# Optimization experiments

Hardware: AMD Instinct MI355X
Metric: run time of the kernel (lower is better)

The kernel has to match this reference:

```python
import jax, jax.numpy as jnp
import numpy as np

GROUPS = 8
EPS = 1e-5


def group_norm(x, w, b, groups=GROUPS, eps=EPS):
    B, C, H, W = x.shape
    xg = x.reshape(B, groups, C // groups, H, W)
    mean = xg.mean(axis=(2, 3, 4), keepdims=True)
    var = xg.var(axis=(2, 3, 4), keepdims=True)
    xg = (xg - mean) * jax.lax.rsqrt(var + eps)
    x = xg.reshape(B, C, H, W)
    return x * w[None, :, None, None] + b[None, :, None, None]


def setup_inputs() -> dict:
    key = jax.random.key(0)
    ks = jax.random.split(key, 7)
    C = 512
    x = jax.random.normal(ks[0], (16, C, 32, 32), dtype=jnp.float32)
    norm_w = jnp.ones((C,), dtype=jnp.float32)
    norm_b = jnp.zeros((C,), dtype=jnp.float32)
    s = 1.0 / np.sqrt(C)
    qkv_w = jax.random.uniform(ks[1], (3 * C, C), jnp.float32, -s, s)
    qkv_b = jax.random.uniform(ks[2], (3 * C,), jnp.float32, -s, s)
    proj_w = jax.random.uniform(ks[3], (C, C), jnp.float32, -s, s)
    proj_b = jax.random.uniform(ks[4], (C,), jnp.float32, -s, s)
    return {"x": x, "norm_w": norm_w, "norm_b": norm_b, "qkv_w": qkv_w,
            "qkv_b": qkv_b, "proj_w": proj_w, "proj_b": proj_b}


def reference(x, norm_w, norm_b, qkv_w, qkv_b, proj_w, proj_b):
    B, C, H, W = x.shape
    h_in = x
    xn = group_norm(x, norm_w, norm_b)
    # 1x1 conv == per-pixel linear over channels
    qkv = jnp.einsum('oc,bchw->bohw', qkv_w, xn) + qkv_b[None, :, None, None]
    q, k, v = jnp.split(qkv, 3, axis=1)
    q = q.reshape(B, C, H * W)
    k = k.reshape(B, C, H * W)
    v = v.reshape(B, C, H * W)
    attn = jnp.einsum('bci,bcj->bij', q, k) / jnp.sqrt(jnp.asarray(C, x.dtype))
    attn = jax.nn.softmax(attn, axis=-1)
    out = jnp.einsum('bij,bcj->bci', attn, v).reshape(B, C, H, W)
    out = jnp.einsum('oc,bchw->bohw', proj_w, out) + proj_b[None, :, None, None]
    return h_in + out
```

## Files before the change

### kernel.cpp

```cpp
#include <hip/hip_runtime.h>
#include <stdint.h>

typedef __attribute__((ext_vector_type(4))) float f32x4;
typedef __attribute__((ext_vector_type(8))) __bf16 bf16x8;

__device__ __forceinline__ unsigned short f2bf(float f) {
  union { float f; unsigned u; } v; v.f = f;
  unsigned r = v.u + 0x7FFF + ((v.u >> 16) & 1);
  return (unsigned short)(r >> 16);
}

__device__ __forceinline__ void g2l16(const void* g, void* l) {
  __builtin_amdgcn_global_load_lds((const __attribute__((address_space(1))) void*)g,
                                   (__attribute__((address_space(3))) void*)l, 16, 0, 0);
}

__global__ void cvt_weights(const float* __restrict__ a, const float* __restrict__ p,
                            unsigned short* __restrict__ wa, unsigned short* __restrict__ wp) {
  int i = blockIdx.x * 256 + threadIdx.x;
  if (i < 786432) wa[i] = f2bf(a[i]);
  else wp[i - 786432] = f2bf(p[i - 786432]);
}

__global__ __launch_bounds__(256) void gn_fused(
    const float* __restrict__ x, const float* __restrict__ gw, const float* __restrict__ gb,
    unsigned short* __restrict__ xnT) {
  __shared__ float tile[64][65];
  __shared__ float red[8];
  __shared__ float mv[2];
  int bid = blockIdx.x;
  int g = bid & 7, b = bid >> 3;
  int t = threadIdx.x;
  const float4* p = (const float4*)(x + (size_t)bid * 65536);
  float s = 0.f, ss = 0.f;
  for (int i = t; i < 16384; i += 256) {
    float4 v = p[i];
    s += v.x + v.y + v.z + v.w;
    ss += v.x * v.x + v.y * v.y + v.z * v.z + v.w * v.w;
  }
#pragma unroll
  for (int o = 32; o > 0; o >>= 1) {
    s += __shfl_down(s, o, 64);
    ss += __shfl_down(ss, o, 64);
  }
  int w = t >> 6;
  if ((t & 63) == 0) { red[w] = s; red[4 + w] = ss; }
  __syncthreads();
  if (t == 0) {
    s = red[0] + red[1] + red[2] + red[3];
    ss = red[4] + red[5] + red[6] + red[7];
    float mean = s * (1.f / 65536.f);
    float var = ss * (1.f / 65536.f) - mean * mean;
    mv[0] = mean; mv[1] = rsqrtf(var + 1e-5f);
  }
  __syncthreads();
  float mean = mv[0], rstd = mv[1];
  const float* src = x + (size_t)bid * 65536;
  for (int ch = 0; ch < 16; ch++) {
#pragma unroll
    for (int i = 0; i < 4; i++) {
      int lin = t + i * 256;
      int c = lin >> 4, p4 = lin & 15;
      float4 v = *(const float4*)(src + (size_t)c * 1024 + ch * 64 + p4 * 4);
      float gg = gw[g * 64 + c] * rstd;
      float bb = gb[g * 64 + c] - mean * gg;
      tile[c][p4 * 4 + 0] = v.x * gg + bb;
      tile[c][p4 * 4 + 1] = v.y * gg + bb;
      tile[c][p4 * 4 + 2] = v.z * gg + bb;
      tile[c][p4 * 4 + 3] = v.w * gg + bb;
    }
    __syncthreads();
    unsigned short* dst = xnT + ((size_t)b * 1024 + ch * 64) * 512 + g * 64;
#pragma unroll
    for (int i = 0; i < 4; i++) {
      int lin = t + i * 256;
      int pp = lin >> 4, cq = lin & 15;
      ushort4 o;
      o.x = f2bf(tile[cq * 4 + 0][pp]);
      o.y = f2bf(tile[cq * 4 + 1][pp]);
      o.z = f2bf(tile[cq * 4 + 2][pp]);
      o.w = f2bf(tile[cq * 4 + 3][pp]);
      *(ushort4*)(dst + (size_t)pp * 512 + cq * 4) = o;
    }
    __syncthreads();
  }
}

template <int EPI, bool OUT_BF16>
__global__ __launch_bounds__(256) void gemm_bt(
    const unsigned short* __restrict__ A, int lda, long long sA,
    const unsigned short* __restrict__ B, int ldb, long long sB,
    void* __restrict__ Cv, int ldc, long long sC,
    const float* __restrict__ bias,
    const float* __restrict__ res, long long sRes,
    int M, int N, int K, int mt, int nt) {
  __shared__ __align__(16) unsigned short As[128 * 32];
  __shared__ __align__(16) unsigned short Bs[128 * 32];
  int bid = blockIdx.x;
  int per = mt * nt;
  int b = bid / per;
  int r = bid % per;
  int mi = r / nt, ni = r % nt;
  int t = threadIdx.x;
  int l = t & 63, w = t >> 6;
  int wm = w >> 1, wn = w & 1;
  int fr = l & 15;
  int fk = (l >> 4) << 3;
  const unsigned short* Ab = A + (size_t)b * sA + (size_t)(mi * 128) * lda;
  const unsigned short* Bb = B + (size_t)b * sB + (size_t)(ni * 128) * ldb;
  int sr = t >> 2, sk = (t & 3) << 3;
  const unsigned short* gA = Ab + (size_t)sr * lda + sk;
  const unsigned short* gB = Bb + (size_t)sr * ldb + sk;
  unsigned short* lA = As + w * 512;
  unsigned short* lB = Bs + w * 512;
  const unsigned short* ra = As + (wm * 64 + fr) * 32 + fk;
  const unsigned short* rb = Bs + (wn * 64 + fr) * 32 + fk;
  f32x4 acc[4][4] = {};
  for (int k0 = 0; k0 < K; k0 += 32) {
    g2l16(gA, lA);
    g2l16(gA + (size_t)64 * lda, lA + 2048);
    g2l16(gB, lB);
    g2l16(gB + (size_t)64 * ldb, lB + 2048);
    gA += 32; gB += 32;
    __syncthreads();
    bf16x8 af[4], bv[4];
#pragma unroll
    for (int i = 0; i < 4; i++) af[i] = *(const bf16x8*)(ra + i * 512);
#pragma unroll
    for (int j = 0; j < 4; j++) bv[j] = *(const bf16x8*)(rb + j * 512);
#pragma unroll
    for (int i = 0; i < 4; i++)
#pragma unroll
      for (int j = 0; j < 4; j++)
        acc[i][j] = __builtin_amdgcn_mfma_f32_16x16x32_bf16(af[i], bv[j], acc[i][j], 0, 0, 0);
    __syncthreads();
  }
  int crow0 = mi * 128 + wm * 64;
  int ccol0 = ni * 128 + wn * 64;
  int lr = (l >> 4) << 2;
  int lc = l & 15;
#pragma unroll
  for (int i = 0; i < 4; i++) {
#pragma unroll
    for (int j = 0; j < 4; j++) {
      int col = ccol0 + j * 16 + lc;
      float bn = (EPI == 1) ? bias[col] : 0.0f;
#pragma unroll
      for (int e = 0; e < 4; e++) {
        int row = crow0 + i * 16 + lr + e;
        float v = acc[i][j][e];
        if (EPI == 1) v += bn;
        if (EPI == 2 || EPI == 3) v += bias[row];
        if (EPI == 3) v += res[(size_t)b * sRes + (size_t)row * ldc + col];
        size_t o = (size_t)b * sC + (size_t)row * ldc + col;
        if (OUT_BF16) ((unsigned short*)Cv)[o] = f2bf(v);
        else ((float*)Cv)[o] = v;
      }
    }
  }
}

__global__ __launch_bounds__(512, 2) void flash_attn(
    const unsigned short* __restrict__ qkT, const unsigned short* __restrict__ vbuf,
    unsigned short* __restrict__ obuf) {
  __shared__ __align__(16) unsigned short Qs[64 * 520];
  __shared__ __align__(16) float Slds[64 * 132];
  __shared__ __align__(16) unsigned short Plds[4 * 64 * 40];
  __shared__ float mrow[64], lrow[64], scl[64];

  const float SC = 0.04419417382415922f;
  int bid = blockIdx.x;
  int logical = (bid & 7) * 32 + (bid >> 3);
  int b = logical >> 4, it = logical & 15;
  int i0 = it * 64;
  int tid = threadIdx.x;
  int l = tid & 63, w = tid >> 6;
  int fr = l & 15, fq = l >> 4;
  int d0 = w * 64;

  const size_t bq = (size_t)b * 1048576;
  const size_t bv = (size_t)b * 524288;

  {
    const unsigned short* qsrc = qkT + bq + (size_t)i0 * 1024 + l * 8;
#pragma unroll
    for (int i = 0; i < 8; i++) {
      int row = i * 8 + w;
      g2l16(qsrc + (size_t)row * 1024, (char*)Qs + row * 1040);
    }
  }
  if (tid < 64) { mrow[tid] = -3e38f; lrow[tid] = 0.f; }
  __syncthreads();

  f32x4 acc[4][4] = {};
  const unsigned short* kg = qkT + bq + 512 + (size_t)(w * 16 + fr) * 1024 + fq * 8;
  const unsigned short* vg = vbuf + bv + (size_t)(d0 + fr) * 1024 + fq * 8;

  int smr = w * 8 + (l & 7);
  int sm8 = l >> 3;

#pragma unroll 1
  for (int jt = 0; jt < 8; jt++) {
    const unsigned short* kgj = kg + (size_t)jt * 131072;
    bf16x8 kf[16];
#pragma unroll
    for (int ks = 0; ks < 16; ks++) kf[ks] = *(const bf16x8*)(kgj + ks * 32);
    const unsigned short* vgj = vg + jt * 128;
    bf16x8 vf[16];
#pragma unroll
    for (int nj = 0; nj < 4; nj++)
#pragma unroll
      for (int kp = 0; kp < 4; kp++)
        vf[nj * 4 + kp] = *(const bf16x8*)(vgj + nj * 16384 + kp * 32);

    {
      f32x4 sacc[4] = {};
#pragma unroll
      for (int ks = 0; ks < 16; ks++) {
#pragma unroll
        for (int mi = 0; mi < 4; mi++) {
          bf16x8 qa = *(const bf16x8*)((const char*)Qs + (mi * 16 + fr) * 1040 + (ks * 4 + fq) * 16);
          sacc[mi] = __builtin_amdgcn_mfma_f32_16x16x32_bf16(qa, kf[ks], sacc[mi], 0, 0, 0);
        }
      }
#pragma unroll
      for (int mi = 0; mi < 4; mi++) {
        float* sp = Slds + (mi * 16 + fq * 4) * 132 + w * 16 + fr;
#pragma unroll
        for (int e = 0; e < 4; e++) sp[e * 132] = sacc[mi][e];
      }
    }
    asm volatile("s_waitcnt lgkmcnt(0)" ::: "memory");
    __builtin_amdgcn_s_barrier();
    __builtin_amdgcn_sched_barrier(0);

    {
      int r = smr, s8 = sm8;
      const float* srowp = Slds + r * 132 + s8 * 16;
      float4 a0 = *(const float4*)(srowp + 0);
      float4 a1 = *(const float4*)(srowp + 4);
      float4 a2 = *(const float4*)(srowp + 8);
      float4 a3 = *(const float4*)(srowp + 12);
      float mx = fmaxf(fmaxf(fmaxf(a0.x, a0.y), fmaxf(a0.z, a0.w)),
                       fmaxf(fmaxf(a1.x, a1.y), fmaxf(a1.z, a1.w)));
      mx = fmaxf(mx, fmaxf(fmaxf(fmaxf(a2.x, a2.y), fmaxf(a2.z, a2.w)),
                           fmaxf(fmaxf(a3.x, a3.y), fmaxf(a3.z, a3.w))));
      mx = fmaxf(mx, __shfl_xor(mx, 8, 64));
      mx = fmaxf(mx, __shfl_xor(mx, 16, 64));
      mx = fmaxf(mx, __shfl_xor(mx, 32, 64));
      float mold = mrow[r];
      float mnew = fmaxf(mold, mx);
      float e0 = __expf((a0.x - mnew) * SC), e1 = __expf((a0.y - mnew) * SC);
      float e2 = __expf((a0.z - mnew) * SC), e3 = __expf((a0.w - mnew) * SC);
      float e4 = __expf((a1.x - mnew) * SC), e5 = __expf((a1.y - mnew) * SC);
      float e6 = __expf((a1.z - mnew) * SC), e7 = __expf((a1.w - mnew) * SC);
      float e8 = __expf((a2.x - mnew) * SC), e9 = __expf((a2.y - mnew) * SC);
      float ea = __expf((a2.z - mnew) * SC), eb = __expf((a2.w - mnew) * SC);
      float ec = __expf((a3.x - mnew) * SC), ed = __expf((a3.y - mnew) * SC);
      float ee = __expf((a3.z - mnew) * SC), ef = __expf((a3.w - mnew) * SC);
      float sum = ((e0 + e1) + (e2 + e3)) + ((e4 + e5) + (e6 + e7)) +
                  ((e8 + e9) + (ea + eb)) + ((ec + ed) + (ee + ef));
      sum += __shfl_xor(sum, 8, 64);
      sum += __shfl_xor(sum, 16, 64);
      sum += __shfl_xor(sum, 32, 64);
      uint4 pw0, pw1;
      pw0.x = f2bf(e0) | ((unsigned)f2bf(e1) << 16);
      pw0.y = f2bf(e2) | ((unsigned)f2bf(e3) << 16);
      pw0.z = f2bf(e4) | ((unsigned)f2bf(e5) << 16);
      pw0.w = f2bf(e6) | ((unsigned)f2bf(e7) << 16);
      pw1.x = f2bf(e8) | ((unsigned)f2bf(e9) << 16);
      pw1.y = f2bf(ea) | ((unsigned)f2bf(eb) << 16);
      pw1.z = f2bf(ec) | ((unsigned)f2bf(ed) << 16);
      pw1.w = f2bf(ee) | ((unsigned)f2bf(ef) << 16);
      char* pp = (char*)Plds + (s8 >> 1) * 5120 + r * 80 + (s8 & 1) * 32;
      *(uint4*)pp = pw0;
      *(uint4*)(pp + 16) = pw1;
      if (s8 == 0) {
        float sf = __expf((mold - mnew) * SC);
        lrow[r] = lrow[r] * sf + sum;
        mrow[r] = mnew;
        scl[r] = sf;
      }
    }
    asm volatile("s_waitcnt lgkmcnt(0)" ::: "memory");
    __builtin_amdgcn_s_barrier();
    __builtin_amdgcn_sched_barrier(0);

    {
      f32x4 sc4[4];
#pragma unroll
      for (int mi = 0; mi < 4; mi++) sc4[mi] = *(const f32x4*)(scl + mi * 16 + fq * 4);
#pragma unroll
      for (int mi = 0; mi < 4; mi++)
#pragma unroll
        for (int nj = 0; nj < 4; nj++) acc[mi][nj] *= sc4[mi];
#pragma unroll
      for (int kp = 0; kp < 4; kp++) {
        bf16x8 pf[4];
#pragma unroll
        for (int mi = 0; mi < 4; mi++)
          pf[mi] = *(const bf16x8*)((const char*)Plds + kp * 5120 + (mi * 16 + fr) * 80 + fq * 16);
#pragma unroll
        for (int nj = 0; nj < 4; nj++) {
#pragma unroll
          for (int mi = 0; mi < 4; mi++)
            acc[mi][nj] = __builtin_amdgcn_mfma_f32_16x16x32_bf16(pf[mi], vf[nj * 4 + kp], acc[mi][nj], 0, 0, 0);
        }
      }
    }
  }

  f32x4 linv[4];
#pragma unroll
  for (int mi = 0; mi < 4; mi++) {
    f32x4 lv = *(const f32x4*)(lrow + mi * 16 + fq * 4);
#pragma unroll
    for (int e = 0; e < 4; e++) linv[mi][e] = 1.0f / lv[e];
  }
  unsigned short* ob = obuf + bv + (size_t)i0 * 512 + d0 + fr;
#pragma unroll
  for (int mi = 0; mi < 4; mi++)
#pragma unroll
    for (int nj = 0; nj < 4; nj++)
#pragma unroll
      for (int e = 0; e < 4; e++) {
        int row = mi * 16 + fq * 4 + e;
        ob[(size_t)row * 512 + nj * 16] = f2bf(acc[mi][nj][e] * linv[mi][e]);
      }
}

extern "C" void kernel_launch(void* const* d_in, const int* in_sizes, int n_in,
                              void* d_out, int out_size, void* d_ws, size_t ws_size,
                              hipStream_t stream) {
  const float* x = (const float*)d_in[0];
  const float* norm_w = (const float*)d_in[1];
  const float* norm_b = (const float*)d_in[2];
  const float* qkv_w = (const float*)d_in[3];
  const float* qkv_b = (const float*)d_in[4];
  const float* proj_w = (const float*)d_in[5];
  const float* proj_b = (const float*)d_in[6];
  float* out = (float*)d_out;
  char* ws = (char*)d_ws;

  size_t off = 0;
  auto alloc = [&](size_t bytes) {
    off = (off + 255) & ~(size_t)255;
    size_t r = off; off += bytes; return r;
  };
  unsigned short* wqkv  = (unsigned short*)(ws + alloc((size_t)1536 * 512 * 2));
  unsigned short* wproj = (unsigned short*)(ws + alloc((size_t)512 * 512 * 2));
  unsigned short* xnT   = (unsigned short*)(ws + alloc((size_t)16 * 1024 * 512 * 2));
  unsigned short* qkT   = (unsigned short*)(ws + alloc((size_t)16 * 1024 * 1024 * 2));
  unsigned short* vbuf  = (unsigned short*)(ws + alloc((size_t)16 * 512 * 1024 * 2));
  unsigned short* obuf  = (unsigned short*)(ws + alloc((size_t)16 * 1024 * 512 * 2));

  cvt_weights<<<4096, 256, 0, stream>>>(qkv_w, proj_w, wqkv, wproj);
  gn_fused<<<128, 256, 0, stream>>>(x, norm_w, norm_b, xnT);

  gemm_bt<1, true><<<1024, 256, 0, stream>>>(
      xnT, 512, 1024LL * 512, wqkv, 512, 0,
      qkT, 1024, 1024LL * 1024, qkv_b, nullptr, 0, 1024, 1024, 512, 8, 8);

  gemm_bt<2, true><<<512, 256, 0, stream>>>(
      wqkv + (size_t)1024 * 512, 512, 0, xnT, 512, 1024LL * 512,
      vbuf, 1024, 512LL * 1024, qkv_b + 1024, nullptr, 0, 512, 1024, 512, 4, 8);

  flash_attn<<<256, 512, 0, stream>>>(qkT, vbuf, obuf);

  gemm_bt<3, false><<<512, 256, 0, stream>>>(
      wproj, 512, 0, obuf, 512, 1024LL * 512,
      out, 1024, 512LL * 1024, proj_b, x, 512LL * 1024, 512, 1024, 512, 4, 8);
}
```

Baseline: 285.3 us.

## Compute flash-attention softmax in registers with per-wave max/sum tables

The softmax no longer goes through an fp32 score tile in LDS. Each wave reduces row maxima and row sums of its own MFMA score fragments with cross-lane shuffles and publishes partials to small double-buffered LDS tables, while running max and sum stay in registers. P is written to LDS directly from the fragments, and the V loads are issued before the K loads. This removes the fp32 score round trip through LDS and the separate softmax thread mapping, at the cost of more shuffles and some redundant exponentials and table reads per lane.

```diff
diff --git a/kernel.cpp b/kernel.cpp
--- a/kernel.cpp
+++ b/kernel.cpp
@@ -164,9 +164,9 @@
     const unsigned short* __restrict__ qkT, const unsigned short* __restrict__ vbuf,
     unsigned short* __restrict__ obuf) {
   __shared__ __align__(16) unsigned short Qs[64 * 520];
-  __shared__ __align__(16) float Slds[64 * 132];
-  __shared__ __align__(16) unsigned short Plds[4 * 64 * 40];
-  __shared__ float mrow[64], lrow[64], scl[64];
+  __shared__ __align__(16) unsigned short Plds[2][64 * 136];
+  __shared__ __align__(16) float mtab[2][8][64];
+  __shared__ __align__(16) float ltab[2][8][64];
 
   const float SC = 0.04419417382415922f;
   int bid = blockIdx.x;
@@ -189,144 +189,136 @@
       g2l16(qsrc + (size_t)row * 1024, (char*)Qs + row * 1040);
     }
   }
-  if (tid < 64) { mrow[tid] = -3e38f; lrow[tid] = 0.f; }
   __syncthreads();
 
   f32x4 acc[4][4] = {};
+  f32x4 mrun[4], lrun[4];
+#pragma unroll
+  for (int mi = 0; mi < 4; mi++) {
+    mrun[mi] = f32x4{-3e38f, -3e38f, -3e38f, -3e38f};
+    lrun[mi] = f32x4{0.f, 0.f, 0.f, 0.f};
+  }
+
   const unsigned short* kg = qkT + bq + 512 + (size_t)(w * 16 + fr) * 1024 + fq * 8;
   const unsigned short* vg = vbuf + bv + (size_t)(d0 + fr) * 1024 + fq * 8;
 
-  int smr = w * 8 + (l & 7);
-  int sm8 = l >> 3;
-
 #pragma unroll 1
   for (int jt = 0; jt < 8; jt++) {
+    int buf = jt & 1;
+    const unsigned short* vgj = vg + jt * 128;
+    bf16x8 vf[16];
+#pragma unroll
+    for (int nj = 0; nj < 4; nj++)
+#pragma unroll
+      for (int kp = 0; kp < 4; kp++)
+        vf[nj * 4 + kp] = *(const bf16x8*)(vgj + nj * 16384 + kp * 32);
+    __builtin_amdgcn_sched_barrier(0);
+
     const unsigned short* kgj = kg + (size_t)jt * 131072;
     bf16x8 kf[16];
 #pragma unroll
     for (int ks = 0; ks < 16; ks++) kf[ks] = *(const bf16x8*)(kgj + ks * 32);
-    const unsigned short* vgj = vg + jt * 128;
-    bf16x8 vf[16];
-#pragma unroll
-    for (int nj = 0; nj < 4; nj++)
-#pragma unroll
-      for (int kp = 0; kp < 4; kp++)
-        vf[nj * 4 + kp] = *(const bf16x8*)(vgj + nj * 16384 + kp * 32);
-
-    {
-      f32x4 sacc[4] = {};
-#pragma unroll
-      for (int ks = 0; ks < 16; ks++) {
-#pragma unroll
-        for (int mi = 0; mi < 4; mi++) {
-          bf16x8 qa = *(const bf16x8*)((const char*)Qs + (mi * 16 + fr) * 1040 + (ks * 4 + fq) * 16);
-          sacc[mi] = __builtin_amdgcn_mfma_f32_16x16x32_bf16(qa, kf[ks], sacc[mi], 0, 0, 0);
-        }
-      }
+    f32x4 sacc[4] = {};
+#pragma unroll
+    for (int ks = 0; ks < 16; ks++) {
 #pragma unroll
       for (int mi = 0; mi < 4; mi++) {
-        float* sp = Slds + (mi * 16 + fq * 4) * 132 + w * 16 + fr;
-#pragma unroll
-        for (int e = 0; e < 4; e++) sp[e * 132] = sacc[mi][e];
-      }
+        bf16x8 qa = *(const bf16x8*)((const char*)Qs + (mi * 16 + fr) * 1040 + (ks * 4 + fq) * 16);
+        sacc[mi] = __builtin_amdgcn_mfma_f32_16x16x32_bf16(qa, kf[ks], sacc[mi], 0, 0, 0);
+      }
+    }
+
+#pragma unroll
+    for (int mi = 0; mi < 4; mi++) {
+      f32x4 v = sacc[mi];
+#pragma unroll
+      for (int mask = 1; mask < 16; mask <<= 1)
+#pragma unroll
+        for (int e = 0; e < 4; e++) v[e] = fmaxf(v[e], __shfl_xor(v[e], mask, 64));
+      if (fr == 0) *(f32x4*)&mtab[buf][w][mi * 16 + fq * 4] = v;
     }
     asm volatile("s_waitcnt lgkmcnt(0)" ::: "memory");
     __builtin_amdgcn_s_barrier();
     __builtin_amdgcn_sched_barrier(0);
 
+    f32x4 alpha[4];
+#pragma unroll
+    for (int mi = 0; mi < 4; mi++) {
+      f32x4 mm = mrun[mi];
+#pragma unroll
+      for (int s = 0; s < 8; s++) {
+        f32x4 ms = *(const f32x4*)&mtab[buf][s][mi * 16 + fq * 4];
+#pragma unroll
+        for (int e = 0; e < 4; e++) mm[e] = fmaxf(mm[e], ms[e]);
+      }
+#pragma unroll
+      for (int e = 0; e < 4; e++) alpha[mi][e] = __expf((mrun[mi][e] - mm[e]) * SC);
+      f32x4 p;
+#pragma unroll
+      for (int e = 0; e < 4; e++) p[e] = __expf((sacc[mi][e] - mm[e]) * SC);
+      sacc[mi] = p;
+      mrun[mi] = mm;
+      f32x4 sum = p;
+#pragma unroll
+      for (int mask = 1; mask < 16; mask <<= 1)
+#pragma unroll
+        for (int e = 0; e < 4; e++) sum[e] += __shfl_xor(sum[e], mask, 64);
+      if (fr == 0) *(f32x4*)&ltab[buf][w][mi * 16 + fq * 4] = sum;
+    }
     {
-      int r = smr, s8 = sm8;
-      const float* srowp = Slds + r * 132 + s8 * 16;
-      float4 a0 = *(const float4*)(srowp + 0);
-      float4 a1 = *(const float4*)(srowp + 4);
-      float4 a2 = *(const float4*)(srowp + 8);
-      float4 a3 = *(const float4*)(srowp + 12);
-      float mx = fmaxf(fmaxf(fmaxf(a0.x, a0.y), fmaxf(a0.z, a0.w)),
-                       fmaxf(fmaxf(a1.x, a1.y), fmaxf(a1.z, a1.w)));
-      mx = fmaxf(mx, fmaxf(fmaxf(fmaxf(a2.x, a2.y), fmaxf(a2.z, a2.w)),
-                           fmaxf(fmaxf(a3.x, a3.y), fmaxf(a3.z, a3.w))));
-      mx = fmaxf(mx, __shfl_xor(mx, 8, 64));
-      mx = fmaxf(mx, __shfl_xor(mx, 16, 64));
-      mx = fmaxf(mx, __shfl_xor(mx, 32, 64));
-      float mold = mrow[r];
-      float mnew = fmaxf(mold, mx);
-      float e0 = __expf((a0.x - mnew) * SC), e1 = __expf((a0.y - mnew) * SC);
-      float e2 = __expf((a0.z - mnew) * SC), e3 = __expf((a0.w - mnew) * SC);
-      float e4 = __expf((a1.x - mnew) * SC), e5 = __expf((a1.y - mnew) * SC);
-      float e6 = __expf((a1.z - mnew) * SC), e7 = __expf((a1.w - mnew) * SC);
-      float e8 = __expf((a2.x - mnew) * SC), e9 = __expf((a2.y - mnew) * SC);
-      float ea = __expf((a2.z - mnew) * SC), eb = __expf((a2.w - mnew) * SC);
-      float ec = __expf((a3.x - mnew) * SC), ed = __expf((a3.y - mnew) * SC);
-      float ee = __expf((a3.z - mnew) * SC), ef = __expf((a3.w - mnew) * SC);
-      float sum = ((e0 + e1) + (e2 + e3)) + ((e4 + e5) + (e6 + e7)) +
-                  ((e8 + e9) + (ea + eb)) + ((ec + ed) + (ee + ef));
-      sum += __shfl_xor(sum, 8, 64);
-      sum += __shfl_xor(sum, 16, 64);
-      sum += __shfl_xor(sum, 32, 64);
-      uint4 pw0, pw1;
-      pw0.x = f2bf(e0) | ((unsigned)f2bf(e1) << 16);
-      pw0.y = f2bf(e2) | ((unsigned)f2bf(e3) << 16);
-      pw0.z = f2bf(e4) | ((unsigned)f2bf(e5) << 16);
-      pw0.w = f2bf(e6) | ((unsigned)f2bf(e7) << 16);
-      pw1.x = f2bf(e8) | ((unsigned)f2bf(e9) << 16);
-      pw1.y = f2bf(ea) | ((unsigned)f2bf(eb) << 16);
-      pw1.z = f2bf(ec) | ((unsigned)f2bf(ed) << 16);
-      pw1.w = f2bf(ee) | ((unsigned)f2bf(ef) << 16);
-      char* pp = (char*)Plds + (s8 >> 1) * 5120 + r * 80 + (s8 & 1) * 32;
-      *(uint4*)pp = pw0;
-      *(uint4*)(pp + 16) = pw1;
-      if (s8 == 0) {
-        float sf = __expf((mold - mnew) * SC);
-        lrow[r] = lrow[r] * sf + sum;
-        mrow[r] = mnew;
-        scl[r] = sf;
-      }
+      unsigned short* pb = &Plds[buf][0] + (fq * 4) * 136 + w * 16 + fr;
+#pragma unroll
+      for (int mi = 0; mi < 4; mi++)
+#pragma unroll
+        for (int e = 0; e < 4; e++)
+          pb[(mi * 16 + e) * 136] = f2bf(sacc[mi][e]);
     }
     asm volatile("s_waitcnt lgkmcnt(0)" ::: "memory");
     __builtin_amdgcn_s_barrier();
     __builtin_amdgcn_sched_barrier(0);
 
-    {
-      f32x4 sc4[4];
-#pragma unroll
-      for (int mi = 0; mi < 4; mi++) sc4[mi] = *(const f32x4*)(scl + mi * 16 + fq * 4);
+#pragma unroll
+    for (int mi = 0; mi < 4; mi++) {
+      f32x4 ls = {0.f, 0.f, 0.f, 0.f};
+#pragma unroll
+      for (int s = 0; s < 8; s++) {
+        f32x4 lv = *(const f32x4*)&ltab[buf][s][mi * 16 + fq * 4];
+#pragma unroll
+        for (int e = 0; e < 4; e++) ls[e] += lv[e];
+      }
+#pragma unroll
+      for (int e = 0; e < 4; e++) lrun[mi][e] = lrun[mi][e] * alpha[mi][e] + ls[e];
+#pragma unroll
+      for (int nj = 0; nj < 4; nj++) acc[mi][nj] *= alpha[mi];
+    }
+#pragma unroll
+    for (int kp = 0; kp < 4; kp++) {
+      bf16x8 pf[4];
 #pragma unroll
       for (int mi = 0; mi < 4; mi++)
-#pragma unroll
-        for (int nj = 0; nj < 4; nj++) acc[mi][nj] *= sc4[mi];
-#pragma unroll
-      for (int kp = 0; kp < 4; kp++) {
-        bf16x8 pf[4];
+        pf[mi] = *(const bf16x8*)(&Plds[buf][0] + (mi * 16 + fr) * 136 + kp * 32 + fq * 8);
+#pragma unroll
+      for (int nj = 0; nj < 4; nj++)
 #pragma unroll
         for (int mi = 0; mi < 4; mi++)
-          pf[mi] = *(const bf16x8*)((const char*)Plds + kp * 5120 + (mi * 16 + fr) * 80 + fq * 16);
-#pragma unroll
-        for (int nj = 0; nj < 4; nj++) {
-#pragma unroll
-          for (int mi = 0; mi < 4; mi++)
-            acc[mi][nj] = __builtin_amdgcn_mfma_f32_16x16x32_bf16(pf[mi], vf[nj * 4 + kp], acc[mi][nj], 0, 0, 0);
-        }
-      }
-    }
-  }
-
-  f32x4 linv[4];
+          acc[mi][nj] = __builtin_amdgcn_mfma_f32_16x16x32_bf16(pf[mi], vf[nj * 4 + kp], acc[mi][nj], 0, 0, 0);
+    }
+  }
+
+  unsigned short* ob = obuf + bv + (size_t)i0 * 512 + d0 + fr;
 #pragma unroll
   for (int mi = 0; mi < 4; mi++) {
-    f32x4 lv = *(const f32x4*)(lrow + mi * 16 + fq * 4);
-#pragma unroll
-    for (int e = 0; e < 4; e++) linv[mi][e] = 1.0f / lv[e];
-  }
-  unsigned short* ob = obuf + bv + (size_t)i0 * 512 + d0 + fr;
-#pragma unroll
-  for (int mi = 0; mi < 4; mi++)
+    f32x4 linv;
+#pragma unroll
+    for (int e = 0; e < 4; e++) linv[e] = 1.0f / lrun[mi][e];
 #pragma unroll
     for (int nj = 0; nj < 4; nj++)
 #pragma unroll
       for (int e = 0; e < 4; e++) {
         int row = mi * 16 + fq * 4 + e;
-        ob[(size_t)row * 512 + nj * 16] = f2bf(acc[mi][nj][e] * linv[mi][e]);
-      }
+        ob[(size_t)row * 512 + nj * 16] = f2bf(acc[mi][nj][e] * linv[e]);
+      }
+  }
 }
 
 extern "C" void kernel_launch(void* const* d_in, const int* in_sizes, int n_in,
```

Result: slower. 329.8 us (+15.6%).
